# Kernel tuning notes

Hardware: AMD Instinct MI355X
Metric: run time of the kernel (lower is better)

Reference implementation:

```python
import jax, jax.numpy as jnp
import numpy as np

D_MODEL = 2048
NHEAD = 16
D_K = D_MODEL // NHEAD


def setup_inputs() -> dict:
    key = jax.random.key(0)
    ks = jax.random.split(key, 11)
    N, S, E = 2, 2048, D_MODEL
    scale = 1.0 / np.sqrt(E)
    inp = {
        "query": jax.random.normal(ks[0], (N, S, E), jnp.float32),
        "key": jax.random.normal(ks[1], (N, S, E), jnp.float32),
        "value": jax.random.normal(ks[2], (N, S, E), jnp.float32),
        "Wq": jax.random.normal(ks[3], (E, E), jnp.float32) * scale,
        "bq": jnp.zeros((E,), jnp.float32),
        "Wk": jax.random.normal(ks[4], (E, E), jnp.float32) * scale,
        "bk": jnp.zeros((E,), jnp.float32),
        "Wv": jax.random.normal(ks[5], (E, E), jnp.float32) * scale,
        "bv": jnp.zeros((E,), jnp.float32),
        "Wo": jax.random.normal(ks[6], (E, E), jnp.float32) * scale,
        "bo": jnp.zeros((E,), jnp.float32),
    }
    return inp


def reference(query, key, value, Wq, bq, Wk, bk, Wv, bv, Wo, bo):
    N, S, E = query.shape
    H, Dk = NHEAD, D_K
    # torch Linear: x @ W.T + b
    q = query @ Wq.T + bq
    k = key @ Wk.T + bk
    v = value @ Wv.T + bv
    # (N, S, E) -> (N, H, S, Dk)
    q = q.reshape(N, S, H, Dk).transpose(0, 2, 1, 3)
    k = k.reshape(N, S, H, Dk).transpose(0, 2, 1, 3)
    v = v.reshape(N, S, H, Dk).transpose(0, 2, 1, 3)
    scores = jnp.einsum('nhsd,nhtd->nhst', q, k) / jnp.sqrt(jnp.float32(Dk))
    attn = jax.nn.softmax(scores, axis=-1)
    out = jnp.einsum('nhst,nhtd->nhsd', attn, v)  # (N, H, S, Dk)
    # FAITHFUL to source bug: direct view (N,H,S,Dk)->(N,S,H*Dk) without head transpose
    out = out.reshape(N, S, H * Dk)
    return out @ Wo.T + bo
```

## Files before the change

### kernel.cpp

```cpp
#include <hip/hip_runtime.h>


typedef __attribute__((ext_vector_type(8))) short bf16x8;
typedef __attribute__((ext_vector_type(4))) short bf16x4;
typedef __attribute__((ext_vector_type(4))) float f32x4;

__device__ __forceinline__ unsigned short f2bf(float f) {
    unsigned u = __float_as_uint(f);
    u += 0x7fffu + ((u >> 16) & 1u);
    return (unsigned short)(u >> 16);
}

__device__ __forceinline__ void gload_lds16(const unsigned short* g, unsigned short* l) {
    __builtin_amdgcn_global_load_lds(
        (const __attribute__((address_space(1))) unsigned int*)g,
        (__attribute__((address_space(3))) unsigned int*)l, 16, 0, 0);
}

__global__ void cvt2(const float* __restrict__ s0, unsigned short* __restrict__ d0, int c0,
                     const float* __restrict__ s1, unsigned short* __restrict__ d1, int c1)
{
    int total = c0 + c1;
    for (int i = blockIdx.x * blockDim.x + threadIdx.x; i < total; i += gridDim.x * blockDim.x) {
        const float* s; unsigned short* d; int j;
        if (i < c0) { s = s0; d = d0; j = i; } else { s = s1; d = d1; j = i - c0; }
        float4 a = ((const float4*)s)[j * 2];
        float4 b = ((const float4*)s)[j * 2 + 1];
        bf16x8 r;
        r[0] = (short)f2bf(a.x); r[1] = (short)f2bf(a.y);
        r[2] = (short)f2bf(a.z); r[3] = (short)f2bf(a.w);
        r[4] = (short)f2bf(b.x); r[5] = (short)f2bf(b.y);
        r[6] = (short)f2bf(b.z); r[7] = (short)f2bf(b.w);
        ((bf16x8*)d)[j] = r;
    }
}

template<int MODE>
__global__ __launch_bounds__(256, 2) void gemm_bt2(
    const unsigned short* __restrict__ A, const unsigned short* __restrict__ B,
    const float* __restrict__ bias, void* __restrict__ Cout, float cscale)
{
    const int K = 2048;
    __shared__ __align__(16) unsigned short SM[32768];

    const int tid  = threadIdx.x;
    const int lane = tid & 63;
    const int w    = tid >> 6;
    const int wr   = w >> 1, wc = w & 1;

    int bid = blockIdx.x;
    int bl  = (bid & 7) * 64 + (bid >> 3);
    const int m0 = (bl & 31) << 7;
    const int n0 = (bl >> 5) << 7;

    const int lr8 = lane >> 3;
    const int sc8 = (lane & 7) ^ lr8;

    f32x4 acc[4][4];
    #pragma unroll
    for (int i = 0; i < 4; ++i)
        #pragma unroll
        for (int j = 0; j < 4; ++j) { f32x4 z = {0.f,0.f,0.f,0.f}; acc[i][j] = z; }

    auto stage = [&](int kt, unsigned short* As_, unsigned short* Bs_) {
        const int k0 = kt * 64;
        #pragma unroll
        for (int i = 0; i < 4; ++i) {
            int row = w * 32 + i * 8 + lr8;
            gload_lds16(A + (size_t)(m0 + row) * K + k0 + sc8 * 8, As_ + (w * 4 + i) * 512);
            gload_lds16(B + (size_t)(n0 + row) * K + k0 + sc8 * 8, Bs_ + (w * 4 + i) * 512);
        }
    };

    stage(0, SM, SM + 8192);
    __syncthreads();

    int cur = 0;
    for (int kt = 0; kt < 32; ++kt) {
        unsigned short* As_ = SM + (cur ? 16384 : 0);
        unsigned short* Bs_ = As_ + 8192;
        if (kt < 31) stage(kt + 1, SM + (cur ? 0 : 16384), SM + (cur ? 8192 : 24576));

        #pragma unroll
        for (int kk = 0; kk < 2; ++kk) {
            const int kc = kk * 32 + (lane >> 4) * 8;
            bf16x8 af[4], bfr[4];
            #pragma unroll
            for (int t = 0; t < 4; ++t) {
                int ar = wr * 64 + t * 16 + (lane & 15);
                af[t]  = *(const bf16x8*)&As_[ar * 64 + (kc ^ ((ar & 7) << 3))];
                int br = wc * 64 + t * 16 + (lane & 15);
                bfr[t] = *(const bf16x8*)&Bs_[br * 64 + (kc ^ ((br & 7) << 3))];
            }
            #pragma unroll
            for (int tm = 0; tm < 4; ++tm)
                #pragma unroll
                for (int tn = 0; tn < 4; ++tn)
                    acc[tm][tn] = __builtin_amdgcn_mfma_f32_16x16x32_bf16(
                        af[tm], bfr[tn], acc[tm][tn], 0, 0, 0);
        }
        __syncthreads();
        cur ^= 1;
    }

    const int lr = lane >> 4, lc = lane & 15;
    #pragma unroll
    for (int tn = 0; tn < 4; ++tn) {
        int col = n0 + wc * 64 + tn * 16 + lc;
        float bv = bias[col];
        #pragma unroll
        for (int tm = 0; tm < 4; ++tm) {
            int row0 = m0 + wr * 64 + tm * 16 + lr * 4;
            if constexpr (MODE == 1) {
                #pragma unroll
                for (int r = 0; r < 4; ++r)
                    ((float*)Cout)[(size_t)(row0 + r) * 2048 + col] = acc[tm][tn][r] + bv;
            } else if constexpr (MODE == 0) {
                #pragma unroll
                for (int r = 0; r < 4; ++r) {
                    int row = row0 + r;
                    int nb = row >> 11, s = row & 2047, h = col >> 7, d = col & 127;
                    ((unsigned short*)Cout)[(((size_t)(nb * 16 + h)) * 2048 + s) * 128 + d] =
                        f2bf((acc[tm][tn][r] + bv) * cscale);
                }
            } else {
                int nb = row0 >> 11, s0 = row0 & 2047, h = col >> 7, d = col & 127;
                bf16x4 pk;
                #pragma unroll
                for (int r = 0; r < 4; ++r) pk[r] = (short)f2bf(acc[tm][tn][r] + bv);
                *(bf16x4*)&((unsigned short*)Cout)[(((size_t)(nb * 16 + h)) * 128 + d) * 2048 + s0] = pk;
            }
        }
    }
}

__global__ __launch_bounds__(256, 2) void attn_fwd2(
    const unsigned short* __restrict__ Qb, const unsigned short* __restrict__ Kb,
    const unsigned short* __restrict__ Vtb, unsigned short* __restrict__ Ob)
{
    __shared__ __align__(16) unsigned short SM[40960];
    unsigned short* Ps     = SM + 32768;
    unsigned short* Qstage = SM + 16384;

    const int tid = threadIdx.x, lane = tid & 63, w = tid >> 6;
    int bid = blockIdx.x;
    int bl  = (bid & 7) * 64 + (bid >> 3);
    const int qt = bl & 15;
    const int hb = bl >> 4;

    const unsigned short* qg  = Qb  + ((size_t)hb * 2048 + qt * 128) * 128;
    const unsigned short* kgb = Kb  + (size_t)hb * 2048 * 128;
    const unsigned short* vgb = Vtb + (size_t)hb * 128 * 2048;

    const int lK_r = lane >> 4, lK_c = lane & 15;
    const int lV_r = lane >> 3, lV_c = lane & 7;

    auto stageKV = [&](int kt, unsigned short* Kc, unsigned short* Vc) {
        #pragma unroll
        for (int i = 0; i < 4; ++i) {
            int ci = w * 4 + i;
            int krow = ci * 4 + lK_r;
            int ksrc = lK_c ^ (krow & 7);
            gload_lds16(kgb + (size_t)(kt * 64 + krow) * 128 + ksrc * 8, Kc + ci * 512);
            int vrow = ci * 8 + lV_r;
            int vsrc = lV_c ^ (vrow & 7);
            gload_lds16(vgb + (size_t)vrow * 2048 + kt * 64 + vsrc * 8, Vc + ci * 512);
        }
    };

    {
        int c = tid & 15, rq = tid >> 4;
        #pragma unroll
        for (int i = 0; i < 8; ++i) {
            int row = i * 16 + rq;
            bf16x8 v = *(const bf16x8*)(qg + row * 128 + c * 8);
            *(bf16x8*)&Qstage[row * 128 + ((c * 8) ^ ((row & 7) << 3))] = v;
        }
    }
    stageKV(0, SM, SM + 8192);
    __syncthreads();

    bf16x8 qf[2][4];
    #pragma unroll
    for (int rg = 0; rg < 2; ++rg) {
        int qrow = w * 32 + rg * 16 + (lane & 15);
        #pragma unroll
        for (int kk = 0; kk < 4; ++kk) {
            int kc = kk * 32 + (lane >> 4) * 8;
            qf[rg][kk] = *(const bf16x8*)&Qstage[qrow * 128 + (kc ^ ((qrow & 7) << 3))];
        }
    }
    __syncthreads();

    f32x4 o[2][8];
    #pragma unroll
    for (int rg = 0; rg < 2; ++rg)
        #pragma unroll
        for (int dt = 0; dt < 8; ++dt) { f32x4 z = {0.f,0.f,0.f,0.f}; o[rg][dt] = z; }
    float mstate[2][4], lstate[2][4];
    #pragma unroll
    for (int rg = 0; rg < 2; ++rg)
        #pragma unroll
        for (int r = 0; r < 4; ++r) { mstate[rg][r] = -INFINITY; lstate[rg][r] = 0.f; }

    int cur = 0;
    for (int kt = 0; kt < 32; ++kt) {
        unsigned short* Kc = SM + (cur ? 16384 : 0);
        unsigned short* Vc = Kc + 8192;
        if (kt < 31) stageKV(kt + 1, SM + (cur ? 0 : 16384), SM + (cur ? 8192 : 24576));

        f32x4 s[2][4];
        #pragma unroll
        for (int rg = 0; rg < 2; ++rg)
            #pragma unroll
            for (int j = 0; j < 4; ++j) { f32x4 z = {0.f,0.f,0.f,0.f}; s[rg][j] = z; }
        __builtin_amdgcn_s_setprio(1);
        #pragma unroll
        for (int kk = 0; kk < 4; ++kk) {
            int kc = kk * 32 + (lane >> 4) * 8;
            #pragma unroll
            for (int j = 0; j < 4; ++j) {
                int krow = j * 16 + (lane & 15);
                bf16x8 kf = *(const bf16x8*)&Kc[krow * 128 + (kc ^ ((krow & 7) << 3))];
                s[0][j] = __builtin_amdgcn_mfma_f32_16x16x32_bf16(qf[0][kk], kf, s[0][j], 0, 0, 0);
                s[1][j] = __builtin_amdgcn_mfma_f32_16x16x32_bf16(qf[1][kk], kf, s[1][j], 0, 0, 0);
            }
        }
        __builtin_amdgcn_s_setprio(0);

        #pragma unroll
        for (int rg = 0; rg < 2; ++rg) {
            float pmax[4];
            #pragma unroll
            for (int r = 0; r < 4; ++r) {
                float v = fmaxf(fmaxf(s[rg][0][r], s[rg][1][r]), fmaxf(s[rg][2][r], s[rg][3][r]));
                v = fmaxf(v, __shfl_xor(v, 1));
                v = fmaxf(v, __shfl_xor(v, 2));
                v = fmaxf(v, __shfl_xor(v, 4));
                v = fmaxf(v, __shfl_xor(v, 8));
                pmax[r] = v;
            }
            bool need = false;
            #pragma unroll
            for (int r = 0; r < 4; ++r) need |= (pmax[r] - mstate[rg][r] > 8.0f);
            if (__any(need)) {
                #pragma unroll
                for (int r = 0; r < 4; ++r) {
                    float nm = fmaxf(mstate[rg][r], pmax[r]);
                    float sc = __expf(mstate[rg][r] - nm);
                    mstate[rg][r] = nm;
                    lstate[rg][r] *= sc;
                    #pragma unroll
                    for (int dt = 0; dt < 8; ++dt) o[rg][dt][r] *= sc;
                }
            }
            float rsum[4] = {0.f, 0.f, 0.f, 0.f};
            #pragma unroll
            for (int j = 0; j < 4; ++j)
                #pragma unroll
                for (int r = 0; r < 4; ++r) {
                    float p = __expf(s[rg][j][r] - mstate[rg][r]);
                    s[rg][j][r] = p;
                    rsum[r] += p;
                }
            #pragma unroll
            for (int r = 0; r < 4; ++r) {
                float t = rsum[r];
                t += __shfl_xor(t, 1);
                t += __shfl_xor(t, 2);
                t += __shfl_xor(t, 4);
                t += __shfl_xor(t, 8);
                lstate[rg][r] += t;
            }
            #pragma unroll
            for (int j = 0; j < 4; ++j)
                #pragma unroll
                for (int r = 0; r < 4; ++r) {
                    int prow = w * 32 + rg * 16 + (lane >> 4) * 4 + r;
                    int pcol = j * 16 + (lane & 15);
                    Ps[prow * 64 + (pcol ^ ((prow & 7) << 3))] = f2bf(s[rg][j][r]);
                }
        }

        __builtin_amdgcn_s_setprio(1);
        #pragma unroll
        for (int kk = 0; kk < 2; ++kk) {
            int kc = kk * 32 + (lane >> 4) * 8;
            int pr0 = w * 32 + (lane & 15);
            bf16x8 pf0 = *(const bf16x8*)&Ps[pr0 * 64 + (kc ^ ((pr0 & 7) << 3))];
            int pr1 = pr0 + 16;
            bf16x8 pf1 = *(const bf16x8*)&Ps[pr1 * 64 + (kc ^ ((pr1 & 7) << 3))];
            #pragma unroll
            for (int dt = 0; dt < 8; ++dt) {
                int vrow = dt * 16 + (lane & 15);
                bf16x8 vf = *(const bf16x8*)&Vc[vrow * 64 + (kc ^ ((vrow & 7) << 3))];
                o[0][dt] = __builtin_amdgcn_mfma_f32_16x16x32_bf16(pf0, vf, o[0][dt], 0, 0, 0);
                o[1][dt] = __builtin_amdgcn_mfma_f32_16x16x32_bf16(pf1, vf, o[1][dt], 0, 0, 0);
            }
        }
        __builtin_amdgcn_s_setprio(0);

        __syncthreads();
        cur ^= 1;
    }

    #pragma unroll
    for (int rg = 0; rg < 2; ++rg)
        #pragma unroll
        for (int r = 0; r < 4; ++r) {
            float inv = 1.0f / lstate[rg][r];
            int qrow = qt * 128 + w * 32 + rg * 16 + (lane >> 4) * 4 + r;
            #pragma unroll
            for (int dt = 0; dt < 8; ++dt)
                Ob[((size_t)hb * 2048 + qrow) * 128 + dt * 16 + (lane & 15)] = f2bf(o[rg][dt][r] * inv);
        }
}

extern "C" void kernel_launch(void* const* d_in, const int* in_sizes, int n_in,
                              void* d_out, int out_size, void* d_ws, size_t ws_size,
                              hipStream_t stream) {
    const float* query = (const float*)d_in[0];
    const float* key   = (const float*)d_in[1];
    const float* value = (const float*)d_in[2];
    const float* Wq    = (const float*)d_in[3];
    const float* bq    = (const float*)d_in[4];
    const float* Wk    = (const float*)d_in[5];
    const float* bk    = (const float*)d_in[6];
    const float* Wv    = (const float*)d_in[7];
    const float* bv    = (const float*)d_in[8];
    const float* Wo    = (const float*)d_in[9];
    const float* bo    = (const float*)d_in[10];

    unsigned short* Qb  = (unsigned short*)d_ws;
    unsigned short* Kb  = Qb  + 8388608;
    unsigned short* Vtb = Kb  + 8388608;
    unsigned short* Xs  = Vtb + 8388608;
    unsigned short* Wsl = (unsigned short*)d_out;
    unsigned short* Wos = Qb;

    const int CX = 1048576;
    const int CW = 524288;
    const float qscale = 0.08838834764831845f;

    dim3 B(256);
    cvt2<<<dim3(1024), B, 0, stream>>>(value, Xs, CX, Wv, Wsl, CW);
    gemm_bt2<2><<<dim3(512), B, 0, stream>>>(Xs, Wsl, bv, Vtb, 1.0f);
    cvt2<<<dim3(1024), B, 0, stream>>>(query, Xs, CX, Wq, Wsl, CW);
    gemm_bt2<0><<<dim3(512), B, 0, stream>>>(Xs, Wsl, bq, Qb, qscale);
    cvt2<<<dim3(1024), B, 0, stream>>>(key, Xs, CX, Wk, Wsl, CW);
    gemm_bt2<0><<<dim3(512), B, 0, stream>>>(Xs, Wsl, bk, Kb, 1.0f);
    attn_fwd2<<<dim3(512), B, 0, stream>>>(Qb, Kb, Vtb, Xs);
    cvt2<<<dim3(512), B, 0, stream>>>(Wo, Wos, CW, Wo, Wos, 0);
    gemm_bt2<1><<<dim3(512), B, 0, stream>>>(Xs, Wos, bo, d_out, 1.0f);
}
```

Measured before the change: 475.3 us.

## Rewrite attention with 32x32 MFMA, register-resident P, and exp2 softmax

Replaces the attention kernel with a 512-thread, 256-query-row variant that computes S^T with 32x32x16 MFMAs. Q fragments are loaded straight from global memory into registers, and the bf16 P tile is passed to the PV MFMA through lane shuffles instead of an LDS round trip. Folds log2(e) into the Q scale so the softmax can use exp2f. The aim is to cut LDS traffic, the P write/read and barriers, and to raise MFMA efficiency, at the cost of more registers per thread and lower occupancy risk.

Result: faster. 456.3 us (-4.0%).

```diff
diff --git a/kernel.cpp b/kernel.cpp
--- a/kernel.cpp
+++ b/kernel.cpp
@@ -4,11 +4,17 @@
 typedef __attribute__((ext_vector_type(8))) short bf16x8;
 typedef __attribute__((ext_vector_type(4))) short bf16x4;
 typedef __attribute__((ext_vector_type(4))) float f32x4;
+typedef __attribute__((ext_vector_type(16))) float f32x16;
+typedef unsigned int u32;
 
 __device__ __forceinline__ unsigned short f2bf(float f) {
     unsigned u = __float_as_uint(f);
     u += 0x7fffu + ((u >> 16) & 1u);
     return (unsigned short)(u >> 16);
+}
+
+__device__ __forceinline__ u32 pack2bf(float lo, float hi) {
+    return (u32)f2bf(lo) | ((u32)f2bf(hi) << 16);
 }
 
 __device__ __forceinline__ void gload_lds16(const unsigned short* g, unsigned short* l) {
@@ -134,186 +140,165 @@
     }
 }
 
-__global__ __launch_bounds__(256, 2) void attn_fwd2(
+__global__ __launch_bounds__(512, 2) void attn_fwd3(
     const unsigned short* __restrict__ Qb, const unsigned short* __restrict__ Kb,
     const unsigned short* __restrict__ Vtb, unsigned short* __restrict__ Ob)
 {
-    __shared__ __align__(16) unsigned short SM[40960];
-    unsigned short* Ps     = SM + 32768;
-    unsigned short* Qstage = SM + 16384;
+    __shared__ __align__(16) unsigned short SM[32768];
 
     const int tid = threadIdx.x, lane = tid & 63, w = tid >> 6;
+    const int l31 = lane & 31, h = lane >> 5;
+
     int bid = blockIdx.x;
-    int bl  = (bid & 7) * 64 + (bid >> 3);
-    const int qt = bl & 15;
-    const int hb = bl >> 4;
-
-    const unsigned short* qg  = Qb  + ((size_t)hb * 2048 + qt * 128) * 128;
+    int bl  = (bid & 7) * 32 + (bid >> 3);
+    const int qt = bl & 7;
+    const int hb = bl >> 3;
+
+    const unsigned short* qg  = Qb  + ((size_t)hb * 2048 + qt * 256) * 128;
     const unsigned short* kgb = Kb  + (size_t)hb * 2048 * 128;
     const unsigned short* vgb = Vtb + (size_t)hb * 128 * 2048;
 
-    const int lK_r = lane >> 4, lK_c = lane & 15;
-    const int lV_r = lane >> 3, lV_c = lane & 7;
-
-    auto stageKV = [&](int kt, unsigned short* Kc, unsigned short* Vc) {
-        #pragma unroll
-        for (int i = 0; i < 4; ++i) {
-            int ci = w * 4 + i;
-            int krow = ci * 4 + lK_r;
-            int ksrc = lK_c ^ (krow & 7);
-            gload_lds16(kgb + (size_t)(kt * 64 + krow) * 128 + ksrc * 8, Kc + ci * 512);
-            int vrow = ci * 8 + lV_r;
-            int vsrc = lV_c ^ (vrow & 7);
-            gload_lds16(vgb + (size_t)vrow * 2048 + kt * 64 + vsrc * 8, Vc + ci * 512);
+    auto stage = [&](int kt, int c) {
+        unsigned short* Kl = SM + c * 16384;
+        unsigned short* Vl = Kl + 8192;
+        #pragma unroll
+        for (int i = 0; i < 2; ++i) {
+            int ck = tid + i * 512;
+            int kr = ck >> 4, kc = (ck & 15) ^ (kr & 15);
+            gload_lds16(kgb + (size_t)(kt * 64 + kr) * 128 + kc * 8, Kl + ck * 8);
+            int cv = tid + i * 512;
+            int vr = cv >> 3, vc = (cv & 7) ^ (vr & 7);
+            gload_lds16(vgb + (size_t)vr * 2048 + kt * 64 + vc * 8, Vl + cv * 8);
         }
     };
 
+    bf16x8 qf[8];
+    const int qrow = qt * 256 + w * 32 + l31;
     {
-        int c = tid & 15, rq = tid >> 4;
-        #pragma unroll
-        for (int i = 0; i < 8; ++i) {
-            int row = i * 16 + rq;
-            bf16x8 v = *(const bf16x8*)(qg + row * 128 + c * 8);
-            *(bf16x8*)&Qstage[row * 128 + ((c * 8) ^ ((row & 7) << 3))] = v;
-        }
-    }
-    stageKV(0, SM, SM + 8192);
+        const unsigned short* qp = Qb + ((size_t)hb * 2048 + qrow) * 128 + h * 8;
+        #pragma unroll
+        for (int ds = 0; ds < 8; ++ds)
+            qf[ds] = *(const bf16x8*)(qp + ds * 16);
+    }
+    (void)qg;
+
+    stage(0, 0);
+
+    f32x16 o[4];
+    #pragma unroll
+    for (int d = 0; d < 4; ++d)
+        #pragma unroll
+        for (int r = 0; r < 16; ++r) o[d][r] = 0.f;
+    float m_ = -INFINITY, l_ = 0.f;
+
     __syncthreads();
 
-    bf16x8 qf[2][4];
+    for (int kt = 0; kt < 32; ++kt) {
+        int cur = kt & 1;
+        if (kt < 31) stage(kt + 1, cur ^ 1);
+        unsigned short* Kl = SM + cur * 16384;
+        unsigned short* Vl = Kl + 8192;
+
+        f32x16 sA, sB;
+        #pragma unroll
+        for (int r = 0; r < 16; ++r) { sA[r] = 0.f; sB[r] = 0.f; }
+        __builtin_amdgcn_s_setprio(1);
+        #pragma unroll
+        for (int ds = 0; ds < 8; ++ds) {
+            int ch = ds * 2 + h;
+            int sw = (ch ^ (l31 & 15)) << 3;
+            bf16x8 k0 = *(const bf16x8*)&Kl[l31 * 128 + sw];
+            bf16x8 k1 = *(const bf16x8*)&Kl[(32 + l31) * 128 + sw];
+            sA = __builtin_amdgcn_mfma_f32_32x32x16_bf16(k0, qf[ds], sA, 0, 0, 0);
+            sB = __builtin_amdgcn_mfma_f32_32x32x16_bf16(k1, qf[ds], sB, 0, 0, 0);
+        }
+        __builtin_amdgcn_s_setprio(0);
+
+        float mx[16];
+        #pragma unroll
+        for (int r = 0; r < 16; ++r) mx[r] = fmaxf(sA[r], sB[r]);
+        #pragma unroll
+        for (int st = 8; st > 0; st >>= 1)
+            #pragma unroll
+            for (int r = 0; r < st; ++r) mx[r] = fmaxf(mx[r], mx[r + st]);
+        float pmax = fmaxf(mx[0], __shfl_xor(mx[0], 32));
+
+        if (__any(pmax - m_ > 8.0f)) {
+            float nm = fmaxf(m_, pmax);
+            float sc = exp2f(m_ - nm);
+            m_ = nm; l_ *= sc;
+            #pragma unroll
+            for (int d = 0; d < 4; ++d)
+                #pragma unroll
+                for (int r = 0; r < 16; ++r) o[d][r] *= sc;
+        }
+
+        float p[32];
+        float sm[16];
+        #pragma unroll
+        for (int r = 0; r < 16; ++r) {
+            p[r]      = exp2f(sA[r] - m_);
+            p[16 + r] = exp2f(sB[r] - m_);
+            sm[r] = p[r] + p[16 + r];
+        }
+        #pragma unroll
+        for (int st = 8; st > 0; st >>= 1)
+            #pragma unroll
+            for (int r = 0; r < st; ++r) sm[r] += sm[r + st];
+        l_ += sm[0] + __shfl_xor(sm[0], 32);
+
+        u32 paw[4][4];
+        #pragma unroll
+        for (int kb = 0; kb < 2; ++kb) {
+            #pragma unroll
+            for (int sg = 0; sg < 2; ++sg) {
+                const int b = kb * 16 + 8 * sg;
+                u32 w0 = pack2bf(p[b + 0], p[b + 1]);
+                u32 w1 = pack2bf(p[b + 2], p[b + 3]);
+                u32 w2 = pack2bf(p[b + 4], p[b + 5]);
+                u32 w3 = pack2bf(p[b + 6], p[b + 7]);
+                u32 s0 = h ? w0 : w2, s1 = h ? w1 : w3;
+                u32 r0 = __shfl_xor(s0, 32), r1 = __shfl_xor(s1, 32);
+                int ks = kb * 2 + sg;
+                paw[ks][0] = h ? r0 : w0;
+                paw[ks][1] = h ? r1 : w1;
+                paw[ks][2] = h ? w2 : r0;
+                paw[ks][3] = h ? w3 : r1;
+            }
+        }
+
+        __builtin_amdgcn_s_setprio(1);
+        #pragma unroll
+        for (int ks = 0; ks < 4; ++ks) {
+            union { u32 u[4]; bf16x8 v; } pu;
+            pu.u[0] = paw[ks][0]; pu.u[1] = paw[ks][1];
+            pu.u[2] = paw[ks][2]; pu.u[3] = paw[ks][3];
+            bf16x8 pa = pu.v;
+            int ch = ks * 2 + h;
+            #pragma unroll
+            for (int db = 0; db < 4; ++db) {
+                int vr = db * 32 + l31;
+                bf16x8 vf = *(const bf16x8*)&Vl[vr * 64 + ((ch ^ (vr & 7)) << 3)];
+                o[db] = __builtin_amdgcn_mfma_f32_32x32x16_bf16(vf, pa, o[db], 0, 0, 0);
+            }
+        }
+        __builtin_amdgcn_s_setprio(0);
+
+        __syncthreads();
+    }
+
+    float inv = 1.0f / l_;
+    unsigned short* op = Ob + ((size_t)hb * 2048 + qrow) * 128;
     #pragma unroll
-    for (int rg = 0; rg < 2; ++rg) {
-        int qrow = w * 32 + rg * 16 + (lane & 15);
-        #pragma unroll
-        for (int kk = 0; kk < 4; ++kk) {
-            int kc = kk * 32 + (lane >> 4) * 8;
-            qf[rg][kk] = *(const bf16x8*)&Qstage[qrow * 128 + (kc ^ ((qrow & 7) << 3))];
-        }
-    }
-    __syncthreads();
-
-    f32x4 o[2][8];
-    #pragma unroll
-    for (int rg = 0; rg < 2; ++rg)
-        #pragma unroll
-        for (int dt = 0; dt < 8; ++dt) { f32x4 z = {0.f,0.f,0.f,0.f}; o[rg][dt] = z; }
-    float mstate[2][4], lstate[2][4];
-    #pragma unroll
-    for (int rg = 0; rg < 2; ++rg)
-        #pragma unroll
-        for (int r = 0; r < 4; ++r) { mstate[rg][r] = -INFINITY; lstate[rg][r] = 0.f; }
-
-    int cur = 0;
-    for (int kt = 0; kt < 32; ++kt) {
-        unsigned short* Kc = SM + (cur ? 16384 : 0);
-        unsigned short* Vc = Kc + 8192;
-        if (kt < 31) stageKV(kt + 1, SM + (cur ? 0 : 16384), SM + (cur ? 8192 : 24576));
-
-        f32x4 s[2][4];
-        #pragma unroll
-        for (int rg = 0; rg < 2; ++rg)
-            #pragma unroll
-            for (int j = 0; j < 4; ++j) { f32x4 z = {0.f,0.f,0.f,0.f}; s[rg][j] = z; }
-        __builtin_amdgcn_s_setprio(1);
-        #pragma unroll
-        for (int kk = 0; kk < 4; ++kk) {
-            int kc = kk * 32 + (lane >> 4) * 8;
-            #pragma unroll
-            for (int j = 0; j < 4; ++j) {
-                int krow = j * 16 + (lane & 15);
-                bf16x8 kf = *(const bf16x8*)&Kc[krow * 128 + (kc ^ ((krow & 7) << 3))];
-                s[0][j] = __builtin_amdgcn_mfma_f32_16x16x32_bf16(qf[0][kk], kf, s[0][j], 0, 0, 0);
-                s[1][j] = __builtin_amdgcn_mfma_f32_16x16x32_bf16(qf[1][kk], kf, s[1][j], 0, 0, 0);
-            }
-        }
-        __builtin_amdgcn_s_setprio(0);
-
-        #pragma unroll
-        for (int rg = 0; rg < 2; ++rg) {
-            float pmax[4];
-            #pragma unroll
-            for (int r = 0; r < 4; ++r) {
-                float v = fmaxf(fmaxf(s[rg][0][r], s[rg][1][r]), fmaxf(s[rg][2][r], s[rg][3][r]));
-                v = fmaxf(v, __shfl_xor(v, 1));
-                v = fmaxf(v, __shfl_xor(v, 2));
-                v = fmaxf(v, __shfl_xor(v, 4));
-                v = fmaxf(v, __shfl_xor(v, 8));
-                pmax[r] = v;
-            }
-            bool need = false;
-            #pragma unroll
-            for (int r = 0; r < 4; ++r) need |= (pmax[r] - mstate[rg][r] > 8.0f);
-            if (__any(need)) {
-                #pragma unroll
-                for (int r = 0; r < 4; ++r) {
-                    float nm = fmaxf(mstate[rg][r], pmax[r]);
-                    float sc = __expf(mstate[rg][r] - nm);
-                    mstate[rg][r] = nm;
-                    lstate[rg][r] *= sc;
-                    #pragma unroll
-                    for (int dt = 0; dt < 8; ++dt) o[rg][dt][r] *= sc;
-                }
-            }
-            float rsum[4] = {0.f, 0.f, 0.f, 0.f};
-            #pragma unroll
-            for (int j = 0; j < 4; ++j)
-                #pragma unroll
-                for (int r = 0; r < 4; ++r) {
-                    float p = __expf(s[rg][j][r] - mstate[rg][r]);
-                    s[rg][j][r] = p;
-                    rsum[r] += p;
-                }
-            #pragma unroll
-            for (int r = 0; r < 4; ++r) {
-                float t = rsum[r];
-                t += __shfl_xor(t, 1);
-                t += __shfl_xor(t, 2);
-                t += __shfl_xor(t, 4);
-                t += __shfl_xor(t, 8);
-                lstate[rg][r] += t;
-            }
-            #pragma unroll
-            for (int j = 0; j < 4; ++j)
-                #pragma unroll
-                for (int r = 0; r < 4; ++r) {
-                    int prow = w * 32 + rg * 16 + (lane >> 4) * 4 + r;
-                    int pcol = j * 16 + (lane & 15);
-                    Ps[prow * 64 + (pcol ^ ((prow & 7) << 3))] = f2bf(s[rg][j][r]);
-                }
-        }
-
-        __builtin_amdgcn_s_setprio(1);
-        #pragma unroll
-        for (int kk = 0; kk < 2; ++kk) {
-            int kc = kk * 32 + (lane >> 4) * 8;
-            int pr0 = w * 32 + (lane & 15);
-            bf16x8 pf0 = *(const bf16x8*)&Ps[pr0 * 64 + (kc ^ ((pr0 & 7) << 3))];
-            int pr1 = pr0 + 16;
-            bf16x8 pf1 = *(const bf16x8*)&Ps[pr1 * 64 + (kc ^ ((pr1 & 7) << 3))];
-            #pragma unroll
-            for (int dt = 0; dt < 8; ++dt) {
-                int vrow = dt * 16 + (lane & 15);
-                bf16x8 vf = *(const bf16x8*)&Vc[vrow * 64 + (kc ^ ((vrow & 7) << 3))];
-                o[0][dt] = __builtin_amdgcn_mfma_f32_16x16x32_bf16(pf0, vf, o[0][dt], 0, 0, 0);
-                o[1][dt] = __builtin_amdgcn_mfma_f32_16x16x32_bf16(pf1, vf, o[1][dt], 0, 0, 0);
-            }
-        }
-        __builtin_amdgcn_s_setprio(0);
-
-        __syncthreads();
-        cur ^= 1;
-    }
-
-    #pragma unroll
-    for (int rg = 0; rg < 2; ++rg)
-        #pragma unroll
-        for (int r = 0; r < 4; ++r) {
-            float inv = 1.0f / lstate[rg][r];
-            int qrow = qt * 128 + w * 32 + rg * 16 + (lane >> 4) * 4 + r;
-            #pragma unroll
-            for (int dt = 0; dt < 8; ++dt)
-                Ob[((size_t)hb * 2048 + qrow) * 128 + dt * 16 + (lane & 15)] = f2bf(o[rg][dt][r] * inv);
-        }
+    for (int db = 0; db < 4; ++db) {
+        #pragma unroll
+        for (int g = 0; g < 4; ++g) {
+            bf16x4 pk;
+            #pragma unroll
+            for (int j = 0; j < 4; ++j) pk[j] = (short)f2bf(o[db][g * 4 + j] * inv);
+            *(bf16x4*)&op[db * 32 + 8 * g + 4 * h] = pk;
+        }
+    }
 }
 
 extern "C" void kernel_launch(void* const* d_in, const int* in_sizes, int n_in,
@@ -340,7 +325,7 @@
 
     const int CX = 1048576;
     const int CW = 524288;
-    const float qscale = 0.08838834764831845f;
+    const float qscale = 0.08838834764831845f * 1.4426950408889634f;
 
     dim3 B(256);
     cvt2<<<dim3(1024), B, 0, stream>>>(value, Xs, CX, Wv, Wsl, CW);
@@ -349,7 +334,7 @@
     gemm_bt2<0><<<dim3(512), B, 0, stream>>>(Xs, Wsl, bq, Qb, qscale);
     cvt2<<<dim3(1024), B, 0, stream>>>(key, Xs, CX, Wk, Wsl, CW);
     gemm_bt2<0><<<dim3(512), B, 0, stream>>>(Xs, Wsl, bk, Kb, 1.0f);
-    attn_fwd2<<<dim3(512), B, 0, stream>>>(Qb, Kb, Vtb, Xs);
+    attn_fwd3<<<dim3(256), dim3(512), 0, stream>>>(Qb, Kb, Vtb, Xs);
     cvt2<<<dim3(512), B, 0, stream>>>(Wo, Wos, CW, Wo, Wos, 0);
     gemm_bt2<1><<<dim3(512), B, 0, stream>>>(Xs, Wos, bo, d_out, 1.0f);
 }
```
